# Kernel optimization log

Measured on AMD Instinct MI355X. Metric: run time of the kernel, lower is better.

The kernel has to match this reference:

```python
import jax, jax.numpy as jnp
import numpy as np
from jax import lax

EPS = 1e-5
DN = ('NCDHW', 'OIDHW', 'NCDHW')
CHANNELS = [4, 32, 64, 128, 256, 512]
OUT_CH = 256


def _conv_s2(x, w):
    # 3x3x3 conv, stride 2, padding 1 (torchsparse spnn.Conv3d on densified grid)
    return lax.conv_general_dilated(x, w, window_strides=(2, 2, 2),
                                    padding=[(1, 1)] * 3, dimension_numbers=DN)


def _bn_relu(x, g, b, m, v):
    # inference BatchNorm (running stats) + ReLU, fused elementwise
    inv = g * lax.rsqrt(v + EPS)           # [C]
    shp = (1, -1, 1, 1, 1)
    return jnp.maximum(x * inv.reshape(shp) + (b - m * inv).reshape(shp), 0.0)


def setup_inputs() -> dict:
    key = jax.random.key(0)
    ks = jax.random.split(key, 32)
    inp = {}
    inp['x'] = jax.random.normal(ks[0], (2, 4, 128, 128, 128), dtype=jnp.float32)
    ki = 1
    for i in range(5):
        cin, cout = CHANNELS[i], CHANNELS[i + 1]
        fan_in = cin * 27
        inp[f'w{i+1}'] = jax.random.normal(ks[ki], (cout, cin, 3, 3, 3), dtype=jnp.float32) / np.sqrt(fan_in); ki += 1
        inp[f'g{i+1}'] = 1.0 + 0.1 * jax.random.normal(ks[ki], (cout,), dtype=jnp.float32); ki += 1
        inp[f'b{i+1}'] = 0.1 * jax.random.normal(ks[ki], (cout,), dtype=jnp.float32); ki += 1
        inp[f'm{i+1}'] = 0.1 * jax.random.normal(ks[ki], (cout,), dtype=jnp.float32); ki += 1
        inp[f'v{i+1}'] = jax.random.uniform(ks[ki], (cout,), dtype=jnp.float32, minval=0.5, maxval=1.5); ki += 1
    inp['w_out'] = jax.random.normal(ks[ki], (OUT_CH, 512, 1, 1, 1), dtype=jnp.float32) / np.sqrt(512.0)
    return inp


def reference(x, w1, g1, b1, m1, v1, w2, g2, b2, m2, v2, w3, g3, b3, m3, v3,
              w4, g4, b4, m4, v4, w5, g5, b5, m5, v5, w_out):
    h = _bn_relu(_conv_s2(x, w1), g1, b1, m1, v1)   # [B,32,64,64,64]
    h = _bn_relu(_conv_s2(h, w2), g2, b2, m2, v2)   # [B,64,32,32,32]
    h = _bn_relu(_conv_s2(h, w3), g3, b3, m3, v3)   # [B,128,16,16,16]
    h = _bn_relu(_conv_s2(h, w4), g4, b4, m4, v4)   # [B,256,8,8,8]
    h = _bn_relu(_conv_s2(h, w5), g5, b5, m5, v5)   # [B,512,4,4,4]
    # 1x1x1 output conv, stride 1
    out = lax.conv_general_dilated(h, w_out, window_strides=(1, 1, 1),
                                   padding=[(0, 0)] * 3, dimension_numbers=DN)
    return out  # [B,256,4,4,4]
```

## Files before the change

kernel.cpp:

```cpp
#include <hip/hip_runtime.h>

static constexpr float kEps = 1e-5f;

using bf16x8 = __attribute__((ext_vector_type(8))) short;
using f32x4 = __attribute__((ext_vector_type(4))) float;

constexpr int ilog2(int n) { return n <= 1 ? 0 : 1 + ilog2(n / 2); }

__device__ inline unsigned bf_rne(float v) {
  unsigned u = __float_as_uint(v);
  return (u + 0x7FFFu + ((u >> 16) & 1u)) >> 16;
}
__device__ inline void split_bf(float v, unsigned short& h, unsigned short& l) {
  unsigned hb = bf_rne(v);
  h = (unsigned short)hb;
  float hf = __uint_as_float(hb << 16);
  l = (unsigned short)bf_rne(v - hf);
}

template <int CIN, int COUT>
__global__ __launch_bounds__(256) void repack_kernel(
    const float* __restrict__ w, const float* __restrict__ g,
    const float* __restrict__ b, const float* __restrict__ m,
    const float* __restrict__ v, float* __restrict__ wT,
    float* __restrict__ bias) {
  int idx = blockIdx.x * 256 + threadIdx.x;
  constexpr int total = COUT * CIN * 27;
  if (idx < COUT) {
    float inv = g[idx] * rsqrtf(v[idx] + kEps);
    bias[idx] = b[idx] - m[idx] * inv;
  }
  if (idx < total) {
    int cout = idx % COUT;
    int ck = idx / COUT;
    int cin = ck / 27;
    int k = ck % 27;
    float inv = g[cout] * rsqrtf(v[cout] + kEps);
    wT[idx] = w[(cout * CIN + cin) * 27 + k] * inv;
  }
}

template <int CIN, int COUT>
__global__ __launch_bounds__(256) void repack_bf16(
    const float* __restrict__ w, const float* __restrict__ g,
    const float* __restrict__ b, const float* __restrict__ m,
    const float* __restrict__ v, unsigned short* __restrict__ wh,
    unsigned short* __restrict__ wl, float* __restrict__ bias) {
  int idx = blockIdx.x * 256 + threadIdx.x;
  constexpr int total = 27 * COUT * CIN;
  constexpr int LC = ilog2(CIN), LO = ilog2(COUT);
  if (idx < COUT) {
    float inv = g[idx] * rsqrtf(v[idx] + kEps);
    bias[idx] = b[idx] - m[idx] * inv;
  }
  if (idx < total) {
    int ci = idx & (CIN - 1);
    int t = idx >> LC;
    int co = t & (COUT - 1);
    int tap = t >> LO;
    float inv = g[co] * rsqrtf(v[co] + kEps);
    float val = w[((size_t)co * CIN + ci) * 27 + tap] * inv;
    unsigned short h, l;
    split_bf(val, h, l);
    wh[idx] = h;
    wl[idx] = l;
  }
}

__global__ __launch_bounds__(256) void repack_wout(const float* __restrict__ w,
                                                   float* __restrict__ wt) {
  int idx = blockIdx.x * 256 + threadIdx.x;
  int co = idx & 255;
  int c = idx >> 8;
  wt[idx] = w[(size_t)co * 512 + c];
}

__global__ __launch_bounds__(256) void conv1_direct(
    const float* __restrict__ in, const float* __restrict__ wT,
    const float* __restrict__ bias, unsigned short* __restrict__ outh,
    unsigned short* __restrict__ outl) {
  constexpr int DI = 128, CIN = 4, COUT = 32;
  int tid = blockIdx.x * 256 + threadIdx.x;
  int x = tid & 63;
  int t = tid >> 6;
  int y = t & 63;
  t >>= 6;
  int z = t & 63;
  int bb = t >> 6;

  float acc[COUT];
#pragma unroll
  for (int i = 0; i < COUT; ++i) acc[i] = 0.f;

  const float* inb = in + (size_t)bb * CIN * DI * DI * DI;
  for (int cin = 0; cin < CIN; ++cin) {
    const float* inc = inb + (size_t)cin * DI * DI * DI;
#pragma unroll
    for (int kz = 0; kz < 3; ++kz) {
      int iz = 2 * z + kz - 1;
      if (iz < 0) continue;
#pragma unroll
      for (int ky = 0; ky < 3; ++ky) {
        int iy = 2 * y + ky - 1;
        if (iy < 0) continue;
        const float* row = inc + ((size_t)iz * DI + iy) * DI;
#pragma unroll
        for (int kx = 0; kx < 3; ++kx) {
          int ix = 2 * x + kx - 1;
          float xv = (ix >= 0) ? row[ix] : 0.f;
          const float* wp = wT + ((size_t)cin * 27 + (kz * 3 + ky) * 3 + kx) * COUT;
#pragma unroll
          for (int i = 0; i < COUT; ++i) acc[i] = fmaf(xv, wp[i], acc[i]);
        }
      }
    }
  }
  size_t op = (size_t)tid * COUT;
#pragma unroll
  for (int i = 0; i < COUT; ++i) {
    float r = fmaxf(acc[i] + bias[i], 0.f);
    unsigned short h, l;
    split_bf(r, h, l);
    outh[op + i] = h;
    outl[op + i] = l;
  }
}

template <int CIN, int COUT, int DO, int SK>
__global__ __launch_bounds__(256) void conv_mfma(
    const unsigned short* __restrict__ inh, const unsigned short* __restrict__ inl,
    const unsigned short* __restrict__ wh, const unsigned short* __restrict__ wl,
    const float* __restrict__ bias, unsigned short* __restrict__ outh,
    unsigned short* __restrict__ outl, float* __restrict__ partial) {
  constexpr int DI = DO * 2;
  constexpr int M = 2 * DO * DO * DO;
  constexpr int TAPS = 27 / SK;
  constexpr int KCPT = CIN / 32;
  constexpr int LD = ilog2(DO);

  const int lane = threadIdx.x & 63;
  const int wv = threadIdx.x >> 6;
  const int mBase = blockIdx.x * 64 + wv * 16;
  const int nBase = blockIdx.y * 64;
  const int skid = blockIdx.z;
  const int mlane = lane & 15;
  const int kgrp = lane >> 4;

  const int m = mBase + mlane;
  const int x = m & (DO - 1);
  const int y = (m >> LD) & (DO - 1);
  const int z = (m >> (2 * LD)) & (DO - 1);
  const int b = m >> (3 * LD);

  f32x4 acc[4] = {{0.f, 0.f, 0.f, 0.f},
                  {0.f, 0.f, 0.f, 0.f},
                  {0.f, 0.f, 0.f, 0.f},
                  {0.f, 0.f, 0.f, 0.f}};

  for (int tp = 0; tp < TAPS; ++tp) {
    const int tap = skid * TAPS + tp;
    const int kz = tap / 9;
    const int kr = tap - kz * 9;
    const int ky = kr / 3;
    const int kx = kr - ky * 3;
    const int iz = 2 * z + kz - 1;
    const int iy = 2 * y + ky - 1;
    const int ix = 2 * x + kx - 1;
    const bool valid = (iz >= 0) && (iy >= 0) && (ix >= 0);
    const size_t aoff =
        ((((size_t)b * DI + iz) * DI + iy) * DI + ix) * CIN + kgrp * 8;
    const unsigned short* ah = inh + aoff;
    const unsigned short* al = inl + aoff;
    const size_t woff = (size_t)tap * COUT * CIN + (size_t)(nBase + mlane) * CIN + kgrp * 8;
    const unsigned short* wbh = wh + woff;
    const unsigned short* wbl = wl + woff;
#pragma unroll
    for (int kc = 0; kc < KCPT; ++kc) {
      bf16x8 Ah = {0, 0, 0, 0, 0, 0, 0, 0};
      bf16x8 Al = {0, 0, 0, 0, 0, 0, 0, 0};
      if (valid) {
        Ah = *reinterpret_cast<const bf16x8*>(ah + kc * 32);
        Al = *reinterpret_cast<const bf16x8*>(al + kc * 32);
      }
#pragma unroll
      for (int nq = 0; nq < 4; ++nq) {
        bf16x8 Bh = *reinterpret_cast<const bf16x8*>(wbh + (size_t)nq * 16 * CIN + kc * 32);
        bf16x8 Bl = *reinterpret_cast<const bf16x8*>(wbl + (size_t)nq * 16 * CIN + kc * 32);
        acc[nq] = __builtin_amdgcn_mfma_f32_16x16x32_bf16(Ah, Bh, acc[nq], 0, 0, 0);
        acc[nq] = __builtin_amdgcn_mfma_f32_16x16x32_bf16(Ah, Bl, acc[nq], 0, 0, 0);
        acc[nq] = __builtin_amdgcn_mfma_f32_16x16x32_bf16(Al, Bh, acc[nq], 0, 0, 0);
      }
    }
  }

  if constexpr (SK == 1) {
#pragma unroll
    for (int nq = 0; nq < 4; ++nq) {
      const int n = nBase + nq * 16 + mlane;
      const float bv = bias[n];
#pragma unroll
      for (int r = 0; r < 4; ++r) {
        const int mrow = mBase + kgrp * 4 + r;
        float vv = fmaxf(acc[nq][r] + bv, 0.f);
        unsigned short h, l;
        split_bf(vv, h, l);
        outh[(size_t)mrow * COUT + n] = h;
        outl[(size_t)mrow * COUT + n] = l;
      }
    }
  } else {
#pragma unroll
    for (int nq = 0; nq < 4; ++nq) {
      const int n = nBase + nq * 16 + mlane;
#pragma unroll
      for (int r = 0; r < 4; ++r) {
        const int mrow = mBase + kgrp * 4 + r;
        partial[((size_t)skid * M + mrow) * COUT + n] = acc[nq][r];
      }
    }
  }
}

template <int COUT, int SK, int M, bool F32OUT>
__global__ __launch_bounds__(256) void reduce_split(
    const float* __restrict__ partial, const float* __restrict__ bias,
    unsigned short* __restrict__ oh, unsigned short* __restrict__ ol,
    float* __restrict__ of) {
  int idx = blockIdx.x * 256 + threadIdx.x;
  int n = idx & (COUT - 1);
  float s = 0.f;
#pragma unroll
  for (int k = 0; k < SK; ++k) s += partial[(size_t)k * M * COUT + idx];
  float v = fmaxf(s + bias[n], 0.f);
  if constexpr (F32OUT) {
    of[idx] = v;
  } else {
    unsigned short h, l;
    split_bf(v, h, l);
    oh[idx] = h;
    ol[idx] = l;
  }
}

__global__ __launch_bounds__(256) void conv1x1_final(
    const float* __restrict__ h5, const float* __restrict__ wt,
    float* __restrict__ out) {
  int p = blockIdx.x;
  int co = threadIdx.x;
  int b = p >> 6;
  int s = p & 63;
  const float* hp = h5 + (size_t)p * 512;
  float acc = 0.f;
#pragma unroll 8
  for (int c = 0; c < 512; ++c) acc = fmaf(hp[c], wt[(size_t)c * 256 + co], acc);
  out[((size_t)b * 256 + co) * 64 + s] = acc;
}

extern "C" void kernel_launch(void* const* d_in, const int* in_sizes, int n_in,
                              void* d_out, int out_size, void* d_ws,
                              size_t ws_size, hipStream_t stream) {
  const float* x = (const float*)d_in[0];
  const float* w1 = (const float*)d_in[1];
  const float* g1 = (const float*)d_in[2];
  const float* bb1 = (const float*)d_in[3];
  const float* m1 = (const float*)d_in[4];
  const float* v1 = (const float*)d_in[5];
  const float* w2 = (const float*)d_in[6];
  const float* g2 = (const float*)d_in[7];
  const float* bb2 = (const float*)d_in[8];
  const float* m2 = (const float*)d_in[9];
  const float* v2 = (const float*)d_in[10];
  const float* w3 = (const float*)d_in[11];
  const float* g3 = (const float*)d_in[12];
  const float* bb3 = (const float*)d_in[13];
  const float* m3 = (const float*)d_in[14];
  const float* v3 = (const float*)d_in[15];
  const float* w4 = (const float*)d_in[16];
  const float* g4 = (const float*)d_in[17];
  const float* bb4 = (const float*)d_in[18];
  const float* m4 = (const float*)d_in[19];
  const float* v4 = (const float*)d_in[20];
  const float* w5 = (const float*)d_in[21];
  const float* g5 = (const float*)d_in[22];
  const float* bb5 = (const float*)d_in[23];
  const float* m5 = (const float*)d_in[24];
  const float* v5 = (const float*)d_in[25];
  const float* w_out = (const float*)d_in[26];
  (void)in_sizes; (void)n_in; (void)out_size; (void)ws_size;

  char* base = (char*)d_ws;
  size_t off = 0;
  auto take = [&](size_t bytes) {
    char* p = base + off;
    off = (off + bytes + 255) & ~(size_t)255;
    return p;
  };
  float* wt1 = (float*)take(3456 * 4);
  unsigned short* w2h = (unsigned short*)take(55296 * 2);
  unsigned short* w2l = (unsigned short*)take(55296 * 2);
  unsigned short* w3h = (unsigned short*)take(221184 * 2);
  unsigned short* w3l = (unsigned short*)take(221184 * 2);
  unsigned short* w4h = (unsigned short*)take(884736 * 2);
  unsigned short* w4l = (unsigned short*)take(884736 * 2);
  unsigned short* w5h = (unsigned short*)take(3538944 * 2);
  unsigned short* w5l = (unsigned short*)take(3538944 * 2);
  float* woutT = (float*)take(131072 * 4);
  float* bs1 = (float*)take(32 * 4);
  float* bs2 = (float*)take(64 * 4);
  float* bs3 = (float*)take(128 * 4);
  float* bs4 = (float*)take(256 * 4);
  float* bs5 = (float*)take(512 * 4);
  unsigned short* h1h = (unsigned short*)take((size_t)16777216 * 2);
  unsigned short* h1l = (unsigned short*)take((size_t)16777216 * 2);
  unsigned short* h2h = (unsigned short*)take((size_t)4194304 * 2);
  unsigned short* h2l = (unsigned short*)take((size_t)4194304 * 2);

  char* AR = (char*)h1h;
  float* p3 = (float*)AR;
  float* p4 = (float*)AR;
  float* p5 = (float*)AR;
  char* AR2 = AR + ((size_t)16 << 20);
  unsigned short* h3h = (unsigned short*)AR2;
  unsigned short* h3l = (unsigned short*)(AR2 + 2097152);
  unsigned short* h4h = (unsigned short*)(AR2 + 2 * 2097152);
  unsigned short* h4l = (unsigned short*)(AR2 + 2 * 2097152 + 524288);
  float* h5 = (float*)(AR2 + 2 * 2097152 + 2 * 524288);

  repack_kernel<4, 32><<<(3456 + 255) / 256, 256, 0, stream>>>(
      w1, g1, bb1, m1, v1, wt1, bs1);
  repack_bf16<32, 64><<<(55296 + 255) / 256, 256, 0, stream>>>(
      w2, g2, bb2, m2, v2, w2h, w2l, bs2);
  repack_bf16<64, 128><<<(221184 + 255) / 256, 256, 0, stream>>>(
      w3, g3, bb3, m3, v3, w3h, w3l, bs3);
  repack_bf16<128, 256><<<(884736 + 255) / 256, 256, 0, stream>>>(
      w4, g4, bb4, m4, v4, w4h, w4l, bs4);
  repack_bf16<256, 512><<<(3538944 + 255) / 256, 256, 0, stream>>>(
      w5, g5, bb5, m5, v5, w5h, w5l, bs5);
  repack_wout<<<512, 256, 0, stream>>>(w_out, woutT);

  conv1_direct<<<2048, 256, 0, stream>>>(x, wt1, bs1, h1h, h1l);

  conv_mfma<32, 64, 32, 1><<<dim3(1024, 1, 1), 256, 0, stream>>>(
      h1h, h1l, w2h, w2l, bs2, h2h, h2l, nullptr);

  conv_mfma<64, 128, 16, 3><<<dim3(128, 2, 3), 256, 0, stream>>>(
      h2h, h2l, w3h, w3l, bs3, nullptr, nullptr, p3);
  reduce_split<128, 3, 8192, false><<<4096, 256, 0, stream>>>(
      p3, bs3, h3h, h3l, nullptr);

  conv_mfma<128, 256, 8, 9><<<dim3(16, 4, 9), 256, 0, stream>>>(
      h3h, h3l, w4h, w4l, bs4, nullptr, nullptr, p4);
  reduce_split<256, 9, 1024, false><<<1024, 256, 0, stream>>>(
      p4, bs4, h4h, h4l, nullptr);

  conv_mfma<256, 512, 4, 9><<<dim3(2, 8, 9), 256, 0, stream>>>(
      h4h, h4l, w5h, w5l, bs5, nullptr, nullptr, p5);
  reduce_split<512, 9, 128, true><<<256, 256, 0, stream>>>(
      p5, bs5, nullptr, nullptr, h5);

  conv1x1_final<<<128, 256, 0, stream>>>(h5, woutT, (float*)d_out);
}
```

Before: 472.3 us.

## Store activations in parity-split layout and add multi-tile M per wave

Activations are now written in a space-to-depth layout split by the parity of z, y and x, so each stride-2 tap reads from a contiguous sub-grid. This aims to make neighbouring output rows read contiguous input rows and improve coalescing. Each wave can now cover MREP 16-row tiles so weight fragments are reused across them. The last layer's split-K grows from 9 to 27 to add parallelism, at the cost of a larger partial buffer, which may not have been enlarged.

```diff
diff --git a/kernel.cpp b/kernel.cpp
--- a/kernel.cpp
+++ b/kernel.cpp
@@ -4,6 +4,7 @@
 
 using bf16x8 = __attribute__((ext_vector_type(8))) short;
 using f32x4 = __attribute__((ext_vector_type(4))) float;
+typedef unsigned short ushort_t;
 
 constexpr int ilog2(int n) { return n <= 1 ? 0 : 1 + ilog2(n / 2); }
 
@@ -115,7 +116,9 @@
       }
     }
   }
-  size_t op = (size_t)tid * COUT;
+  int pidx = (z & 1) * 4 + (y & 1) * 2 + (x & 1);
+  size_t sub = (((size_t)(z >> 1) * 32) + (y >> 1)) * 32 + (x >> 1);
+  size_t op = (((size_t)bb * 8 + pidx) * 32768 + sub) * COUT;
 #pragma unroll
   for (int i = 0; i < COUT; ++i) {
     float r = fmaxf(acc[i] + bias[i], 0.f);
@@ -126,36 +129,41 @@
   }
 }
 
-template <int CIN, int COUT, int DO, int SK>
+template <int CIN, int COUT, int DO, int SK, int MREP>
 __global__ __launch_bounds__(256) void conv_mfma(
     const unsigned short* __restrict__ inh, const unsigned short* __restrict__ inl,
     const unsigned short* __restrict__ wh, const unsigned short* __restrict__ wl,
     const float* __restrict__ bias, unsigned short* __restrict__ outh,
     unsigned short* __restrict__ outl, float* __restrict__ partial) {
-  constexpr int DI = DO * 2;
   constexpr int M = 2 * DO * DO * DO;
   constexpr int TAPS = 27 / SK;
   constexpr int KCPT = CIN / 32;
   constexpr int LD = ilog2(DO);
+  constexpr int SUB = DO * DO * DO;
 
   const int lane = threadIdx.x & 63;
   const int wv = threadIdx.x >> 6;
-  const int mBase = blockIdx.x * 64 + wv * 16;
+  const int mWave = (blockIdx.x * 4 + wv) * (MREP * 16);
   const int nBase = blockIdx.y * 64;
   const int skid = blockIdx.z;
   const int mlane = lane & 15;
   const int kgrp = lane >> 4;
 
-  const int m = mBase + mlane;
-  const int x = m & (DO - 1);
-  const int y = (m >> LD) & (DO - 1);
-  const int z = (m >> (2 * LD)) & (DO - 1);
-  const int b = m >> (3 * LD);
-
-  f32x4 acc[4] = {{0.f, 0.f, 0.f, 0.f},
-                  {0.f, 0.f, 0.f, 0.f},
-                  {0.f, 0.f, 0.f, 0.f},
-                  {0.f, 0.f, 0.f, 0.f}};
+  int xf[MREP], yf[MREP], zf[MREP], bf_[MREP];
+#pragma unroll
+  for (int f = 0; f < MREP; ++f) {
+    int m = mWave + f * 16 + mlane;
+    xf[f] = m & (DO - 1);
+    yf[f] = (m >> LD) & (DO - 1);
+    zf[f] = (m >> (2 * LD)) & (DO - 1);
+    bf_[f] = m >> (3 * LD);
+  }
+
+  f32x4 acc[MREP][4];
+#pragma unroll
+  for (int f = 0; f < MREP; ++f)
+#pragma unroll
+    for (int q = 0; q < 4; ++q) acc[f][q] = (f32x4){0.f, 0.f, 0.f, 0.f};
 
   for (int tp = 0; tp < TAPS; ++tp) {
     const int tap = skid * TAPS + tp;
@@ -163,71 +171,101 @@
     const int kr = tap - kz * 9;
     const int ky = kr / 3;
     const int kx = kr - ky * 3;
-    const int iz = 2 * z + kz - 1;
-    const int iy = 2 * y + ky - 1;
-    const int ix = 2 * x + kx - 1;
-    const bool valid = (iz >= 0) && (iy >= 0) && (ix >= 0);
-    const size_t aoff =
-        ((((size_t)b * DI + iz) * DI + iy) * DI + ix) * CIN + kgrp * 8;
-    const unsigned short* ah = inh + aoff;
-    const unsigned short* al = inl + aoff;
+    const int pidx = (kz != 1) * 4 + (ky != 1) * 2 + (kx != 1);
+    const int dz = (kz == 0), dy = (ky == 0), dx = (kx == 0);
+
     const size_t woff = (size_t)tap * COUT * CIN + (size_t)(nBase + mlane) * CIN + kgrp * 8;
     const unsigned short* wbh = wh + woff;
     const unsigned short* wbl = wl + woff;
+
+    long long aoff[MREP];
+    bool valid[MREP];
+#pragma unroll
+    for (int f = 0; f < MREP; ++f) {
+      int sx = xf[f] - dx, sy = yf[f] - dy, sz = zf[f] - dz;
+      valid[f] = ((sx | sy | sz) >= 0);
+      aoff[f] = ((long long)(bf_[f] * 8 + pidx) * SUB + (sz * DO + sy) * DO + sx) * CIN +
+                kgrp * 8;
+    }
+
 #pragma unroll
     for (int kc = 0; kc < KCPT; ++kc) {
-      bf16x8 Ah = {0, 0, 0, 0, 0, 0, 0, 0};
-      bf16x8 Al = {0, 0, 0, 0, 0, 0, 0, 0};
-      if (valid) {
-        Ah = *reinterpret_cast<const bf16x8*>(ah + kc * 32);
-        Al = *reinterpret_cast<const bf16x8*>(al + kc * 32);
+      bf16x8 Ah[MREP], Al[MREP];
+#pragma unroll
+      for (int f = 0; f < MREP; ++f) {
+        Ah[f] = (bf16x8){0, 0, 0, 0, 0, 0, 0, 0};
+        Al[f] = (bf16x8){0, 0, 0, 0, 0, 0, 0, 0};
+        if (valid[f]) {
+          Ah[f] = *reinterpret_cast<const bf16x8*>(inh + aoff[f] + kc * 32);
+          Al[f] = *reinterpret_cast<const bf16x8*>(inl + aoff[f] + kc * 32);
+        }
       }
 #pragma unroll
       for (int nq = 0; nq < 4; ++nq) {
         bf16x8 Bh = *reinterpret_cast<const bf16x8*>(wbh + (size_t)nq * 16 * CIN + kc * 32);
         bf16x8 Bl = *reinterpret_cast<const bf16x8*>(wbl + (size_t)nq * 16 * CIN + kc * 32);
-        acc[nq] = __builtin_amdgcn_mfma_f32_16x16x32_bf16(Ah, Bh, acc[nq], 0, 0, 0);
-        acc[nq] = __builtin_amdgcn_mfma_f32_16x16x32_bf16(Ah, Bl, acc[nq], 0, 0, 0);
-        acc[nq] = __builtin_amdgcn_mfma_f32_16x16x32_bf16(Al, Bh, acc[nq], 0, 0, 0);
+#pragma unroll
+        for (int f = 0; f < MREP; ++f) {
+          acc[f][nq] = __builtin_amdgcn_mfma_f32_16x16x32_bf16(Ah[f], Bh, acc[f][nq], 0, 0, 0);
+          acc[f][nq] = __builtin_amdgcn_mfma_f32_16x16x32_bf16(Ah[f], Bl, acc[f][nq], 0, 0, 0);
+          acc[f][nq] = __builtin_amdgcn_mfma_f32_16x16x32_bf16(Al[f], Bh, acc[f][nq], 0, 0, 0);
+        }
       }
     }
   }
 
   if constexpr (SK == 1) {
-#pragma unroll
-    for (int nq = 0; nq < 4; ++nq) {
-      const int n = nBase + nq * 16 + mlane;
-      const float bv = bias[n];
-#pragma unroll
-      for (int r = 0; r < 4; ++r) {
-        const int mrow = mBase + kgrp * 4 + r;
-        float vv = fmaxf(acc[nq][r] + bv, 0.f);
-        unsigned short h, l;
-        split_bf(vv, h, l);
-        outh[(size_t)mrow * COUT + n] = h;
-        outl[(size_t)mrow * COUT + n] = l;
+    constexpr int HD = DO / 2;
+#pragma unroll
+    for (int f = 0; f < MREP; ++f) {
+#pragma unroll
+      for (int nq = 0; nq < 4; ++nq) {
+        const int n = nBase + nq * 16 + mlane;
+        const float bv = bias[n];
+#pragma unroll
+        for (int r = 0; r < 4; ++r) {
+          const int mrow = mWave + f * 16 + kgrp * 4 + r;
+          const int ox = mrow & (DO - 1);
+          const int oy = (mrow >> LD) & (DO - 1);
+          const int oz = (mrow >> (2 * LD)) & (DO - 1);
+          const int ob = mrow >> (3 * LD);
+          const int pp = (oz & 1) * 4 + (oy & 1) * 2 + (ox & 1);
+          const size_t sub = (((size_t)(oz >> 1) * HD) + (oy >> 1)) * HD + (ox >> 1);
+          const size_t addr = (((size_t)ob * 8 + pp) * (HD * HD * HD) + sub) * COUT + n;
+          float vv = fmaxf(acc[f][nq][r] + bv, 0.f);
+          unsigned short h, l;
+          split_bf(vv, h, l);
+          outh[addr] = h;
+          outl[addr] = l;
+        }
       }
     }
   } else {
 #pragma unroll
-    for (int nq = 0; nq < 4; ++nq) {
-      const int n = nBase + nq * 16 + mlane;
-#pragma unroll
-      for (int r = 0; r < 4; ++r) {
-        const int mrow = mBase + kgrp * 4 + r;
-        partial[((size_t)skid * M + mrow) * COUT + n] = acc[nq][r];
+    for (int f = 0; f < MREP; ++f) {
+#pragma unroll
+      for (int nq = 0; nq < 4; ++nq) {
+        const int n = nBase + nq * 16 + mlane;
+#pragma unroll
+        for (int r = 0; r < 4; ++r) {
+          const int mrow = mWave + f * 16 + kgrp * 4 + r;
+          partial[((size_t)skid * M + mrow) * COUT + n] = acc[f][nq][r];
+        }
       }
     }
   }
 }
 
-template <int COUT, int SK, int M, bool F32OUT>
+template <int COUT, int SK, int M, int DOP, bool F32OUT>
 __global__ __launch_bounds__(256) void reduce_split(
     const float* __restrict__ partial, const float* __restrict__ bias,
     unsigned short* __restrict__ oh, unsigned short* __restrict__ ol,
     float* __restrict__ of) {
+  constexpr int LD = ilog2(DOP);
+  constexpr int HD = DOP / 2;
   int idx = blockIdx.x * 256 + threadIdx.x;
   int n = idx & (COUT - 1);
+  int mrow = idx / COUT;
   float s = 0.f;
 #pragma unroll
   for (int k = 0; k < SK; ++k) s += partial[(size_t)k * M * COUT + idx];
@@ -235,10 +273,17 @@
   if constexpr (F32OUT) {
     of[idx] = v;
   } else {
+    const int ox = mrow & (DOP - 1);
+    const int oy = (mrow >> LD) & (DOP - 1);
+    const int oz = (mrow >> (2 * LD)) & (DOP - 1);
+    const int ob = mrow >> (3 * LD);
+    const int pp = (oz & 1) * 4 + (oy & 1) * 2 + (ox & 1);
+    const size_t sub = (((size_t)(oz >> 1) * HD) + (oy >> 1)) * HD + (ox >> 1);
+    const size_t addr = (((size_t)ob * 8 + pp) * (HD * HD * HD) + sub) * COUT + n;
     unsigned short h, l;
     split_bf(v, h, l);
-    oh[idx] = h;
-    ol[idx] = l;
+    oh[addr] = h;
+    ol[addr] = l;
   }
 }
 
@@ -340,22 +385,22 @@
 
   conv1_direct<<<2048, 256, 0, stream>>>(x, wt1, bs1, h1h, h1l);
 
-  conv_mfma<32, 64, 32, 1><<<dim3(1024, 1, 1), 256, 0, stream>>>(
+  conv_mfma<32, 64, 32, 1, 2><<<dim3(512, 1, 1), 256, 0, stream>>>(
       h1h, h1l, w2h, w2l, bs2, h2h, h2l, nullptr);
 
-  conv_mfma<64, 128, 16, 3><<<dim3(128, 2, 3), 256, 0, stream>>>(
+  conv_mfma<64, 128, 16, 3, 2><<<dim3(64, 2, 3), 256, 0, stream>>>(
       h2h, h2l, w3h, w3l, bs3, nullptr, nullptr, p3);
-  reduce_split<128, 3, 8192, false><<<4096, 256, 0, stream>>>(
+  reduce_split<128, 3, 8192, 16, false><<<4096, 256, 0, stream>>>(
       p3, bs3, h3h, h3l, nullptr);
 
-  conv_mfma<128, 256, 8, 9><<<dim3(16, 4, 9), 256, 0, stream>>>(
+  conv_mfma<128, 256, 8, 9, 1><<<dim3(16, 4, 9), 256, 0, stream>>>(
       h3h, h3l, w4h, w4l, bs4, nullptr, nullptr, p4);
-  reduce_split<256, 9, 1024, false><<<1024, 256, 0, stream>>>(
+  reduce_split<256, 9, 1024, 8, false><<<1024, 256, 0, stream>>>(
       p4, bs4, h4h, h4l, nullptr);
 
-  conv_mfma<256, 512, 4, 9><<<dim3(2, 8, 9), 256, 0, stream>>>(
+  conv_mfma<256, 512, 4, 27, 1><<<dim3(2, 8, 27), 256, 0, stream>>>(
       h4h, h4l, w5h, w5l, bs5, nullptr, nullptr, p5);
-  reduce_split<512, 9, 128, true><<<256, 256, 0, stream>>>(
+  reduce_split<512, 27, 128, 4, true><<<256, 256, 0, stream>>>(
       p5, bs5, nullptr, nullptr, h5);
 
   conv1x1_final<<<128, 256, 0, stream>>>(h5, woutT, (float*)d_out);
```

Measured after the change: 421.6 us. 10.7% less time.
